# Kernel optimization log

Hardware: AMD Instinct MI355X
Metric: run time of the kernel (lower is better)

The kernel has to match this reference:

```python
import jax, jax.numpy as jnp
import numpy as np

N = 32768        # total nodes (B * max_num_nodes)
E = 524288       # edges, avg degree 16
F_ORI = 32       # data.x_ori feature dim
F_G = 32         # each gamora_output feature dim
IN = F_ORI + 3 * F_G  # 128
H = 256          # hidden_dim
OUT = 16         # out_dim
MAXN = 1024      # max_num_nodes
EPS = 1e-5       # BatchNorm eps


def setup_inputs() -> dict:
    key = jax.random.key(0)
    ks = list(jax.random.split(key, 32))
    g = lambda k, shape, fan: jax.random.normal(k, shape, jnp.float32) / np.sqrt(fan)
    inp = {}
    inp['x_ori'] = jax.random.normal(ks[0], (N, F_ORI), jnp.float32)
    inp['g0'] = jax.random.normal(ks[1], (N, F_G), jnp.float32)
    inp['g1'] = jax.random.normal(ks[2], (N, F_G), jnp.float32)
    inp['g2'] = jax.random.normal(ks[3], (N, F_G), jnp.float32)
    inp['edge_index'] = jax.random.randint(ks[4], (2, E), 0, N, jnp.int64)
    # SAGEConv layer 0: in_dim -> hidden
    inp['Wl0'] = g(ks[5], (IN, H), IN)
    inp['Wr0'] = g(ks[6], (IN, H), IN)
    inp['bb0'] = jnp.zeros((H,), jnp.float32)
    # SAGEConv layers 1..3: hidden -> hidden (stacked)
    inp['Wl'] = g(ks[7], (3, H, H), H)
    inp['Wr'] = g(ks[8], (3, H, H), H)
    inp['bb'] = jnp.zeros((3, H), jnp.float32)
    # BatchNorm per conv layer
    inp['gamma'] = jnp.ones((4, H), jnp.float32)
    inp['beta'] = jnp.zeros((4, H), jnp.float32)
    # mlp1: [max_num_nodes, hidden, 1]
    inp['W1a'] = g(ks[9], (MAXN, H), MAXN)
    inp['b1a'] = jnp.zeros((H,), jnp.float32)
    inp['W1b'] = g(ks[10], (H, 1), H)
    inp['b1b'] = jnp.zeros((1,), jnp.float32)
    # final BatchNorm
    inp['gamma_f'] = jnp.ones((H,), jnp.float32)
    inp['beta_f'] = jnp.zeros((H,), jnp.float32)
    # mlp2: [hidden, hidden, out_dim]
    inp['W2a'] = g(ks[11], (H, H), H)
    inp['b2a'] = jnp.zeros((H,), jnp.float32)
    inp['W2b'] = g(ks[12], (H, OUT), H)
    inp['b2b'] = jnp.zeros((OUT,), jnp.float32)
    return inp


def _bn(x, gamma, beta):
    # training-mode BatchNorm1d over the node/batch axis (biased variance)
    m = jnp.mean(x, axis=0)
    v = jnp.var(x, axis=0)
    return (x - m) * jax.lax.rsqrt(v + EPS) * gamma + beta


def _sage(x, src, dst, inv_deg, Wl, Wr, b):
    # mean neighbor aggregation (gather -> segment_sum -> normalize), then
    # out = lin_l(mean_agg) + lin_r(x)  (PyG SAGEConv, aggr='mean')
    agg = jax.ops.segment_sum(x[src], dst, num_segments=N)
    mean = agg * inv_deg[:, None]
    return mean @ Wl + x @ Wr + b


def reference(x_ori, g0, g1, g2, edge_index, Wl0, Wr0, bb0, Wl, Wr, bb,
              gamma, beta, W1a, b1a, W1b, b1b, gamma_f, beta_f,
              W2a, b2a, W2b, b2b):
    x = jnp.concatenate([x_ori, g0, g1, g2], axis=1)  # [N, IN]
    dst, src = edge_index[0], edge_index[1]
    deg = jax.ops.segment_sum(jnp.ones((E,), x.dtype), dst, num_segments=N)
    inv_deg = jnp.where(deg > 0, 1.0 / jnp.maximum(deg, 1.0), 0.0)
    # layer 0
    x = jax.nn.relu(_bn(_sage(x, src, dst, inv_deg, Wl0, Wr0, bb0), gamma[0], beta[0]))
    # layers 1..3 (dropout is identity in eval-mode reference)
    for i in range(3):
        x = jax.nn.relu(_bn(_sage(x, src, dst, inv_deg, Wl[i], Wr[i], bb[i]),
                            gamma[i + 1], beta[i + 1]))
    x = x.reshape(-1, H, MAXN)                 # [B, H, MAXN]
    h = jax.nn.relu(x @ W1a + b1a)             # [B, H, H]
    x = (h @ W1b + b1b).squeeze(2)             # [B, H]
    x = jax.nn.relu(_bn(x, gamma_f, beta_f))
    x = jax.nn.relu(x @ W2a + b2a) @ W2b + b2b  # [B, OUT]
    return x
```

## Files before the change

### kernel.cpp

```cpp
#include <hip/hip_runtime.h>

#define NN 32768
#define NE 524288
#define HD 256
#define TOTP 794897

#define GAS __attribute__((address_space(1)))
#define LAS __attribute__((address_space(3)))

typedef __attribute__((ext_vector_type(8))) __bf16 bf16x8;
typedef __attribute__((ext_vector_type(4))) float f32x4;

__device__ __forceinline__ float ld_any(const void* p, int i, int isbf16) {
    return isbf16 ? (float)((const __bf16*)p)[i] : ((const float*)p)[i];
}

struct PtrTable { const void* p[18]; };


__global__ __launch_bounds__(256) void k_pre(const unsigned* __restrict__ xw, const int* __restrict__ ei,
                                             PtrTable pt, const void* __restrict__ p0, const void* __restrict__ p1,
                                             const void* __restrict__ p2, const void* __restrict__ p3,
                                             int* __restrict__ flags, int* __restrict__ deg,
                                             __bf16* __restrict__ blob, __bf16* __restrict__ X0c) {
    __shared__ int fl[2];
    const int t = threadIdx.x;
    if (t < 64) {
        unsigned L = xw[t] & 0xFFFFu;
        int e = (int)((L >> 7) & 0xFF);
        unsigned long long b = __ballot(e >= 90 && e <= 135);
        if (t == 0) fl[0] = (b == ~0ULL) ? 1 : 0;
    } else if (t < 128) {
        int u = t - 64;
        unsigned long long b = __ballot(ei[2 * u + 1] != 0);
        if (t == 64) fl[1] = (b == 0ULL) ? 1 : 0;
    }
    __syncthreads();
    const int f0 = fl[0], f1 = fl[1];
    const int blk = blockIdx.x;
    if (blk == 0 && t < 2) flags[t] = fl[t];
    if (blk < 2048) {
        int i0 = (blk * 256 + t) * 8;
        int n = i0 >> 7, f = i0 & 127;
        const void* src = (f < 32) ? p0 : (f < 64) ? p1 : (f < 96) ? p2 : p3;
        int si = n * 32 + (f & 31);
        bf16x8 o;
        #pragma unroll
        for (int j = 0; j < 8; ++j) o[j] = (__bf16)ld_any(src, si + j, f0);
        *(bf16x8*)&X0c[i0] = o;
    } else if (blk < 3601) {
        const int off[23] = {0, 32768, 65536, 65792, 131328, 196864, 262400, 327936, 393472,
                             459008, 459776, 460800, 461824, 723968, 724224, 724480, 724481,
                             724737, 724993, 790529, 790785, 794881, TOTP};
        const signed char pidx[22] = {0, 1, 2, 3, 3, 3, 4, 4, 4, 5, 6, 7, 8, 9, 10, 11, 12, 13, 14, 15, 16, 17};
        const int sbase[22] = {0, 0, 0, 0, 65536, 131072, 0, 65536, 131072, 0, 0, 0, 0, 0, 0, 0, 0, 0, 0, 0, 0, 0};
        const signed char lR[22] = {7, 7, -1, 8, 8, 8, 8, 8, 8, -1, -1, -1, 10, -1, -1, -1, -1, -1, -1, -1, -1, -1};
        const signed char lC[22] = {8, 8, 0, 8, 8, 8, 8, 8, 8, 0, 0, 0, 8, 0, 0, 0, 0, 0, 0, 0, 0, 0};
        int base = ((blk - 2048) * 256 + t) * 2;
        #pragma unroll
        for (int j = 0; j < 2; ++j) {
            int i = base + j;
            if (i >= TOTP) break;
            int s = 0;
            while (i >= off[s + 1]) ++s;
            int jj = i - off[s];
            int si;
            if (lR[s] >= 0) {
                int Rm = (1 << lR[s]) - 1;
                si = sbase[s] + ((jj & Rm) << lC[s]) + (jj >> lR[s]);
            } else {
                si = sbase[s] + jj;
            }
            blob[i] = (__bf16)ld_any(pt.p[pidx[s]], si, f0);
        }
    } else {
        int e0 = ((blk - 3601) * 256 + t) * 2;
        int d0 = f1 ? ei[2 * e0] : ei[e0];
        int d1 = f1 ? ei[2 * e0 + 2] : ei[e0 + 1];
        atomicAdd(&deg[d0], 1);
        atomicAdd(&deg[d1], 1);
    }
}


__global__ __launch_bounds__(256) void k_alloc(const int* __restrict__ deg, int* __restrict__ gcur,
                                               int* __restrict__ offs, float* __restrict__ invd) {
    const int n = blockIdx.x * 256 + threadIdx.x;
    const int lane = threadIdx.x & 63;
    const int v = deg[n];
    invd[n] = v ? 1.f / (float)v : 0.f;
    int incl = v;
    #pragma unroll
    for (int d = 1; d < 64; d <<= 1) {
        int y = __shfl_up(incl, d, 64);
        if (lane >= d) incl += y;
    }
    int base = 0;
    if (lane == 63) base = atomicAdd(gcur, incl);
    base = __shfl(base, 63, 64);
    offs[n] = base + incl - v;
}

__global__ __launch_bounds__(256) void k_fill(const int* __restrict__ ei, const int* __restrict__ flags,
                                              const int* __restrict__ offs, int* __restrict__ cursor,
                                              int* __restrict__ csr) {
    int e = blockIdx.x * 256 + threadIdx.x;
    int f = flags[1];
    int d = f ? ei[2 * e] : ei[e];
    int s = f ? ei[2 * NE + 2 * e] : ei[NE + e];
    int p = atomicAdd(&cursor[d], 1);
    csr[offs[d] + p] = s;
}


__global__ __launch_bounds__(256) void k_agg0(const __bf16* __restrict__ X, const int* __restrict__ csr,
                                              const int* __restrict__ offs, const int* __restrict__ deg,
                                              const float* __restrict__ invd, __bf16* __restrict__ M) {
    const int t = threadIdx.x;
    const int s = blockIdx.x & 1;
    const int n = (blockIdx.x >> 1) * 32 + (t >> 3);
    const int fo = s * 64 + (t & 7) * 8;
    const int beg = offs[n], end = beg + deg[n];
    float a[8] = {};
    for (int e = beg; e < end; e += 8) {
        #pragma unroll
        for (int u = 0; u < 8; ++u) {
            int ee = e + u;
            int idx = csr[ee < end ? ee : end - 1] & (NN - 1);
            float mk = ee < end ? 1.f : 0.f;
            bf16x8 v = *(const bf16x8*)&X[(size_t)idx * 128 + fo];
            #pragma unroll
            for (int j = 0; j < 8; ++j) a[j] += mk * (float)v[j];
        }
    }
    const float id = invd[n];
    bf16x8 o;
    #pragma unroll
    for (int j = 0; j < 8; ++j) o[j] = (__bf16)(a[j] * id);
    *(bf16x8*)&M[(size_t)n * 128 + fo] = o;
}

__global__ __launch_bounds__(256) void k_agg(const __bf16* __restrict__ X, const int* __restrict__ csr,
                                             const int* __restrict__ offs, const int* __restrict__ deg,
                                             const float* __restrict__ invd, __bf16* __restrict__ M) {
    const int t = threadIdx.x;
    const int s = blockIdx.x & 3;
    const int n = (blockIdx.x >> 2) * 32 + (t >> 3);
    const int fo = s * 64 + (t & 7) * 8;
    const int beg = offs[n], end = beg + deg[n];
    float a[8] = {};
    for (int e = beg; e < end; e += 8) {
        #pragma unroll
        for (int u = 0; u < 8; ++u) {
            int ee = e + u;
            int idx = csr[ee < end ? ee : end - 1] & (NN - 1);
            float mk = ee < end ? 1.f : 0.f;
            bf16x8 v = *(const bf16x8*)&X[(size_t)idx * HD + fo];
            #pragma unroll
            for (int j = 0; j < 8; ++j) a[j] += mk * (float)v[j];
        }
    }
    const float id = invd[n];
    bf16x8 o;
    #pragma unroll
    for (int j = 0; j < 8; ++j) o[j] = (__bf16)(a[j] * id);
    *(bf16x8*)&M[(size_t)n * HD + fo] = o;
}


template <int MODE, int TM, int BNA>
__global__ __launch_bounds__(256) void k_gemm(const __bf16* __restrict__ A1, const __bf16* __restrict__ WT1,
                                              const __bf16* __restrict__ A2, const __bf16* __restrict__ WT2,
                                              const __bf16* __restrict__ bias, int KD,
                                              __bf16* __restrict__ O, float* __restrict__ colsum,
                                              const __bf16* __restrict__ W1b, float* __restrict__ x2,
                                              const float* __restrict__ pstatA, const __bf16* __restrict__ gA,
                                              const __bf16* __restrict__ bA) {
    constexpr int MI = TM / 32;
    __shared__ __bf16 As[2][TM][32];
    __shared__ __bf16 Bs[2][128][32];
    __shared__ float scs[256], shs[256];
    const int t = threadIdx.x;
    const int lane = t & 63, w = t >> 6;
    const int wm = w >> 1, wn = w & 1;
    const int quad = lane >> 4, l15 = lane & 15;
    const int row0 = blockIdx.x * TM, c0 = blockIdx.y * 128;
    const int dr = lane >> 2, dc = (lane & 3) * 8;
    if constexpr (BNA != 0) {
        const float invn = 1.0f / NN;
        float m = pstatA[t] * invn;
        float var = fmaxf(pstatA[256 + t] * invn - m * m, 0.f);
        float rs = rsqrtf(var + 1e-5f);
        float g = (float)gA[t] * rs;
        scs[t] = g;
        shs[t] = (float)bA[t] - m * g;
    }
    f32x4 acc[MI][4] = {};
    const int npass = A2 ? 2 : 1;
    for (int pass = 0; pass < npass; ++pass) {
        const __bf16* __restrict__ A = pass ? A2 : A1;
        const __bf16* __restrict__ WT = pass ? WT2 : WT1;
        for (int k0 = 0; k0 < KD; k0 += 64) {
            __syncthreads();
            #pragma unroll
            for (int kk = 0; kk < 2; ++kk) {
                #pragma unroll
                for (int i = 0; i < 2; ++i) {
                    const __bf16* g = &WT[(size_t)(c0 + w * 32 + i * 16 + dr) * KD + k0 + kk * 32 + dc];
                    __builtin_amdgcn_global_load_lds((const GAS void*)g, (LAS void*)&Bs[kk][w * 32 + i * 16][0],
                                                     16, 0, 0);
                }
                if ((BNA >> pass) & 1) {
                    const int kb = (k0 + kk * 32 + dc) & 255;
                    #pragma unroll
                    for (int i = 0; i < TM / 64; ++i) {
                        const __bf16* g = &A[(size_t)(row0 + w * (TM / 4) + i * 16 + dr) * KD + k0 + kk * 32 + dc];
                        bf16x8 v = *(const bf16x8*)g;
                        bf16x8 o;
                        #pragma unroll
                        for (int j = 0; j < 8; ++j)
                            o[j] = (__bf16)fmaxf((float)v[j] * scs[kb + j] + shs[kb + j], 0.f);
                        *(bf16x8*)&As[kk][w * (TM / 4) + i * 16 + dr][dc] = o;
                    }
                } else {
                    #pragma unroll
                    for (int i = 0; i < TM / 64; ++i) {
                        const __bf16* g = &A[(size_t)(row0 + w * (TM / 4) + i * 16 + dr) * KD + k0 + kk * 32 + dc];
                        __builtin_amdgcn_global_load_lds((const GAS void*)g,
                                                         (LAS void*)&As[kk][w * (TM / 4) + i * 16][0], 16, 0, 0);
                    }
                }
            }
            __syncthreads();
            #pragma unroll
            for (int kk = 0; kk < 2; ++kk) {
                bf16x8 af[MI], bfr[4];
                #pragma unroll
                for (int i = 0; i < MI; ++i) af[i] = *(const bf16x8*)&As[kk][wm * (TM / 2) + i * 16 + l15][quad * 8];
                #pragma unroll
                for (int j = 0; j < 4; ++j) bfr[j] = *(const bf16x8*)&Bs[kk][wn * 64 + j * 16 + l15][quad * 8];
                #pragma unroll
                for (int i = 0; i < MI; ++i)
                    #pragma unroll
                    for (int j = 0; j < 4; ++j)
                        acc[i][j] = __builtin_amdgcn_mfma_f32_16x16x32_bf16(af[i], bfr[j], acc[i][j], 0, 0, 0);
            }
        }
    }
    __syncthreads();
    if constexpr (MODE == 0) {
        float* lsum = (float*)&As[0][0][0];
        lsum[t] = 0.f;
        __syncthreads();
        #pragma unroll
        for (int j = 0; j < 4; ++j) {
            const int cb = wn * 64 + j * 16 + l15;
            const int col = c0 + cb;
            const float b = (float)bias[col];
            float s = 0.f, q = 0.f;
            #pragma unroll
            for (int i = 0; i < MI; ++i) {
                const size_t rbase = (size_t)(row0 + wm * (TM / 2) + i * 16 + quad * 4) * HD + col;
                #pragma unroll
                for (int r = 0; r < 4; ++r) {
                    float y = acc[i][j][r] + b;
                    O[rbase + (size_t)r * HD] = (__bf16)y;
                    s += y;
                    q += y * y;
                }
            }
            s += __shfl_xor(s, 16, 64); s += __shfl_xor(s, 32, 64);
            q += __shfl_xor(q, 16, 64); q += __shfl_xor(q, 32, 64);
            if (quad == 0) {
                atomicAdd(&lsum[cb], s);
                atomicAdd(&lsum[128 + cb], q);
            }
        }
        __syncthreads();
        if (t < 128) atomicAdd(&colsum[c0 + t], lsum[t]);
        else atomicAdd(&colsum[256 + c0 + t - 128], lsum[t]);
    } else {
        float bj[4], wj[4];
        #pragma unroll
        for (int j = 0; j < 4; ++j) {
            const int col = c0 + wn * 64 + j * 16 + l15;
            bj[j] = (float)bias[col];
            wj[j] = (float)W1b[col];
        }
        #pragma unroll
        for (int i = 0; i < MI; ++i) {
            #pragma unroll
            for (int r = 0; r < 4; ++r) {
                float p = 0.f;
                #pragma unroll
                for (int j = 0; j < 4; ++j) p += fmaxf(acc[i][j][r] + bj[j], 0.f) * wj[j];
                p += __shfl_xor(p, 1, 64); p += __shfl_xor(p, 2, 64);
                p += __shfl_xor(p, 4, 64); p += __shfl_xor(p, 8, 64);
                if (l15 == 0) atomicAdd(&x2[row0 + wm * (TM / 2) + i * 16 + quad * 4 + r], p);
            }
        }
    }
}


__global__ __launch_bounds__(256) void k_bnapply(__bf16* __restrict__ Y, const float* __restrict__ pstat,
                                                 const __bf16* __restrict__ gamma, const __bf16* __restrict__ beta) {
    __shared__ float sc[256], sh[256];
    const int t = threadIdx.x;
    {
        const float invn = 1.0f / NN;
        float m = pstat[t] * invn;
        float var = fmaxf(pstat[256 + t] * invn - m * m, 0.f);
        float rs = rsqrtf(var + 1e-5f);
        float s = (float)gamma[t] * rs;
        sc[t] = s;
        sh[t] = (float)beta[t] - m * s;
    }
    __syncthreads();
    size_t i = ((size_t)blockIdx.x * 256 + t) * 8;
    int c = (int)(i & 255);
    bf16x8 y = *(const bf16x8*)&Y[i];
    bf16x8 o;
    #pragma unroll
    for (int j = 0; j < 8; ++j) o[j] = (__bf16)fmaxf((float)y[j] * sc[c + j] + sh[c + j], 0.f);
    *(bf16x8*)&Y[i] = o;
}


__global__ __launch_bounds__(256) void k_mlp2(const float* __restrict__ x2, const __bf16* __restrict__ b1b,
                                              const __bf16* __restrict__ gf, const __bf16* __restrict__ bf_,
                                              const __bf16* __restrict__ W2a, const __bf16* __restrict__ b2a,
                                              const __bf16* __restrict__ W2b, const __bf16* __restrict__ b2b,
                                              const int* __restrict__ flags, void* __restrict__ out) {
    __shared__ float row[HD];
    __shared__ float hbuf[HD];
    __shared__ float part[256];
    const int b = blockIdx.x, t = threadIdx.x;
    const float b1 = (float)b1b[0];
    float s = 0.f, q = 0.f, mine = 0.f;
    #pragma unroll
    for (int r = 0; r < 32; ++r) {
        float v = x2[r * HD + t] + b1;
        s += v; q += v * v;
        if (r == b) mine = v;
    }
    float m = s * (1.0f / 32.0f);
    float var = fmaxf(q * (1.0f / 32.0f) - m * m, 0.f);
    float rs = rsqrtf(var + 1e-5f);
    float sc = (float)gf[t] * rs;
    float sh = (float)bf_[t] - m * sc;
    row[t] = fmaxf(mine * sc + sh, 0.f);
    __syncthreads();
    float acc = (float)b2a[t];
    for (int j = 0; j < HD; ++j) acc += row[j] * (float)W2a[j * HD + t];
    hbuf[t] = fmaxf(acc, 0.f);
    __syncthreads();
    const int k = t & 15, g = t >> 4;
    float p = 0.f;
    #pragma unroll
    for (int jj = 0; jj < 16; ++jj) p += hbuf[g * 16 + jj] * (float)W2b[(g * 16 + jj) * 16 + k];
    part[t] = p;
    __syncthreads();
    if (t < 16) {
        float o = (float)b2b[t];
        #pragma unroll
        for (int g2 = 0; g2 < 16; ++g2) o += part[g2 * 16 + t];
        if (flags[0]) ((__bf16*)out)[b * 16 + t] = (__bf16)o;
        else ((float*)out)[b * 16 + t] = o;
    }
}


extern "C" void kernel_launch(void* const* d_in, const int* in_sizes, int n_in,
                              void* d_out, int out_size, void* d_ws, size_t ws_size,
                              hipStream_t stream) {
    const int* ei = (const int*)d_in[4];

    char* ws = (char*)d_ws;
    size_t off_ = 0;
    auto ALLOC = [&](size_t b) { char* p = ws + off_; off_ += (b + 255) & ~(size_t)255; return p; };
    int* flags_ = (int*)ALLOC(8);
    size_t zbeg = off_;
    int* deg_ = (int*)ALLOC(NN * 4);
    int* cursor_ = (int*)ALLOC(NN * 4);
    float* colsum_ = (float*)ALLOC(4 * 512 * 4);
    float* x2_ = (float*)ALLOC(8192 * 4);
    int* gcur_ = (int*)ALLOC(4);
    size_t zlen = off_ - zbeg;
    int* offs_ = (int*)ALLOC(NN * 4);
    float* invd_ = (float*)ALLOC(NN * 4);
    int* csr_ = (int*)ALLOC((size_t)NE * 4);
    __bf16* blob_ = (__bf16*)ALLOC((size_t)TOTP * 2);
    __bf16* M_ = (__bf16*)ALLOC((size_t)NN * HD * 2);
    __bf16* Xa_ = (__bf16*)ALLOC((size_t)NN * HD * 2);
    __bf16* Xb_ = (__bf16*)ALLOC((size_t)NN * HD * 2);
    __bf16* X0c_ = Xb_;

    __bf16* Wl0T = blob_ + 0;
    __bf16* Wr0T = blob_ + 32768;
    __bf16* bb0c = blob_ + 65536;
    __bf16* WlT = blob_ + 65792;
    __bf16* WrT = blob_ + 262400;
    __bf16* bbc = blob_ + 459008;
    __bf16* gammac = blob_ + 459776;
    __bf16* betac = blob_ + 460800;
    __bf16* W1aT = blob_ + 461824;
    __bf16* b1ac = blob_ + 723968;
    __bf16* W1bc = blob_ + 724224;
    __bf16* b1bc = blob_ + 724480;
    __bf16* gfc = blob_ + 724481;
    __bf16* bfc = blob_ + 724737;
    __bf16* W2ac = blob_ + 724993;
    __bf16* b2ac = blob_ + 790529;
    __bf16* W2bc = blob_ + 790785;
    __bf16* b2bc = blob_ + 794881;

    PtrTable pt;
    pt.p[0] = d_in[5];  pt.p[1] = d_in[6];  pt.p[2] = d_in[7];  pt.p[3] = d_in[8];
    pt.p[4] = d_in[9];  pt.p[5] = d_in[10]; pt.p[6] = d_in[11]; pt.p[7] = d_in[12];
    pt.p[8] = d_in[13]; pt.p[9] = d_in[14]; pt.p[10] = d_in[15]; pt.p[11] = d_in[16];
    pt.p[12] = d_in[17]; pt.p[13] = d_in[18]; pt.p[14] = d_in[19]; pt.p[15] = d_in[20];
    pt.p[16] = d_in[21]; pt.p[17] = d_in[22];

    hipMemsetAsync(ws + zbeg, 0, zlen, stream);
    k_pre<<<4625, 256, 0, stream>>>((const unsigned*)d_in[0], ei, pt, d_in[0], d_in[1], d_in[2], d_in[3],
                                    flags_, deg_, blob_, X0c_);
    k_alloc<<<NN / 256, 256, 0, stream>>>(deg_, gcur_, offs_, invd_);
    k_fill<<<NE / 256, 256, 0, stream>>>(ei, flags_, offs_, cursor_, csr_);

    k_agg0<<<NN / 32 * 2, 256, 0, stream>>>(X0c_, csr_, offs_, deg_, invd_, M_);
    k_gemm<0, 128, 0><<<dim3(NN / 128, 2), 256, 0, stream>>>(M_, Wl0T, X0c_, Wr0T, bb0c, 128, Xa_, colsum_,
                                                             nullptr, nullptr, nullptr, nullptr, nullptr);
    k_bnapply<<<NN / 8, 256, 0, stream>>>(Xa_, colsum_, gammac, betac);

    __bf16* Xin = Xa_;
    __bf16* Xo = Xb_;
    for (int l = 0; l < 3; ++l) {
        float* cs = colsum_ + (l + 1) * 512;
        k_agg<<<NN / 32 * 4, 256, 0, stream>>>(Xin, csr_, offs_, deg_, invd_, M_);
        k_gemm<0, 128, 0><<<dim3(NN / 128, 2), 256, 0, stream>>>(M_, WlT + (size_t)l * HD * HD, Xin,
                                                                 WrT + (size_t)l * HD * HD, bbc + l * HD, 256, Xo,
                                                                 cs, nullptr, nullptr, nullptr, nullptr, nullptr);
        if (l < 2) k_bnapply<<<NN / 8, 256, 0, stream>>>(Xo, cs, gammac + (l + 1) * HD, betac + (l + 1) * HD);
        __bf16* tmp = Xin; Xin = Xo; Xo = tmp;
    }

    k_gemm<1, 64, 1><<<dim3(8192 / 64, 2), 256, 0, stream>>>(Xin, W1aT, nullptr, nullptr, b1ac, 1024, nullptr,
                                                             nullptr, W1bc, x2_, colsum_ + 3 * 512,
                                                             gammac + 3 * HD, betac + 3 * HD);
    k_mlp2<<<32, 256, 0, stream>>>(x2_, b1bc, gfc, bfc, W2ac, b2ac, W2bc, b2bc, flags_, d_out);
}
```

Before: 419.1 us.

## Spread edge gathers across wavefront lanes with padded CSR rows

The neighbor aggregation kernels now give each node a full wavefront: four edge groups of 16 lanes each gather 4-wide bf16 feature slices in parallel and combine them with cross-lane shuffles, instead of one 8-thread group walking edges serially. CSR row offsets are padded to multiples of 8 so that edge indices can be read with aligned int4 loads, and the CSR buffer is enlarged to fit the padding. This aims to raise memory-level parallelism and shorten the per-node serial chain. In exchange it launches eight times more blocks, issues smaller loads, and adds shuffle-reduction overhead.

```diff
diff --git a/kernel.cpp b/kernel.cpp
--- a/kernel.cpp
+++ b/kernel.cpp
@@ -9,6 +9,7 @@
 #define LAS __attribute__((address_space(3)))
 
 typedef __attribute__((ext_vector_type(8))) __bf16 bf16x8;
+typedef __attribute__((ext_vector_type(4))) __bf16 bf16x4;
 typedef __attribute__((ext_vector_type(4))) float f32x4;
 
 __device__ __forceinline__ float ld_any(const void* p, int i, int isbf16) {
@@ -89,7 +90,8 @@
     const int lane = threadIdx.x & 63;
     const int v = deg[n];
     invd[n] = v ? 1.f / (float)v : 0.f;
-    int incl = v;
+    const int v8 = (v + 7) & ~7;
+    int incl = v8;
     #pragma unroll
     for (int d = 1; d < 64; d <<= 1) {
         int y = __shfl_up(incl, d, 64);
@@ -98,7 +100,7 @@
     int base = 0;
     if (lane == 63) base = atomicAdd(gcur, incl);
     base = __shfl(base, 63, 64);
-    offs[n] = base + incl - v;
+    offs[n] = base + incl - v8;
 }
 
 __global__ __launch_bounds__(256) void k_fill(const int* __restrict__ ei, const int* __restrict__ flags,
@@ -118,26 +120,50 @@
                                               const float* __restrict__ invd, __bf16* __restrict__ M) {
     const int t = threadIdx.x;
     const int s = blockIdx.x & 1;
-    const int n = (blockIdx.x >> 1) * 32 + (t >> 3);
-    const int fo = s * 64 + (t & 7) * 8;
+    const int n = (blockIdx.x >> 1) * 4 + (t >> 6);
+    const int lane = t & 63;
+    const int eg = lane >> 4;
+    const int fo = s * 64 + (lane & 15) * 4;
     const int beg = offs[n], end = beg + deg[n];
-    float a[8] = {};
-    for (int e = beg; e < end; e += 8) {
-        #pragma unroll
-        for (int u = 0; u < 8; ++u) {
-            int ee = e + u;
-            int idx = csr[ee < end ? ee : end - 1] & (NN - 1);
-            float mk = ee < end ? 1.f : 0.f;
-            bf16x8 v = *(const bf16x8*)&X[(size_t)idx * 128 + fo];
-            #pragma unroll
-            for (int j = 0; j < 8; ++j) a[j] += mk * (float)v[j];
-        }
-    }
-    const float id = invd[n];
-    bf16x8 o;
-    #pragma unroll
-    for (int j = 0; j < 8; ++j) o[j] = (__bf16)(a[j] * id);
-    *(bf16x8*)&M[(size_t)n * 128 + fo] = o;
+    float a0 = 0.f, a1 = 0.f, a2 = 0.f, a3 = 0.f;
+    int e = beg;
+    for (; e + 8 <= end; e += 8) {
+        int4 c0 = *(const int4*)&csr[e];
+        int4 c1 = *(const int4*)&csr[e + 4];
+        int ia = ((eg == 0) ? c0.x : (eg == 1) ? c0.y : (eg == 2) ? c0.z : c0.w) & (NN - 1);
+        int ib = ((eg == 0) ? c1.x : (eg == 1) ? c1.y : (eg == 2) ? c1.z : c1.w) & (NN - 1);
+        bf16x4 va = *(const bf16x4*)&X[(size_t)ia * 128 + fo];
+        bf16x4 vb = *(const bf16x4*)&X[(size_t)ib * 128 + fo];
+        a0 += (float)va[0]; a1 += (float)va[1]; a2 += (float)va[2]; a3 += (float)va[3];
+        a0 += (float)vb[0]; a1 += (float)vb[1]; a2 += (float)vb[2]; a3 += (float)vb[3];
+    }
+    if (e + 4 <= end) {
+        int4 c0 = *(const int4*)&csr[e];
+        int ia = ((eg == 0) ? c0.x : (eg == 1) ? c0.y : (eg == 2) ? c0.z : c0.w) & (NN - 1);
+        bf16x4 va = *(const bf16x4*)&X[(size_t)ia * 128 + fo];
+        a0 += (float)va[0]; a1 += (float)va[1]; a2 += (float)va[2]; a3 += (float)va[3];
+        e += 4;
+    }
+    const int r = end - e;
+    if (r > 0) {
+        int ee = e + (eg < r ? eg : r - 1);
+        int idx = csr[ee] & (NN - 1);
+        float mk = eg < r ? 1.f : 0.f;
+        bf16x4 v = *(const bf16x4*)&X[(size_t)idx * 128 + fo];
+        a0 += mk * (float)v[0]; a1 += mk * (float)v[1];
+        a2 += mk * (float)v[2]; a3 += mk * (float)v[3];
+    }
+    a0 += __shfl_xor(a0, 16, 64); a0 += __shfl_xor(a0, 32, 64);
+    a1 += __shfl_xor(a1, 16, 64); a1 += __shfl_xor(a1, 32, 64);
+    a2 += __shfl_xor(a2, 16, 64); a2 += __shfl_xor(a2, 32, 64);
+    a3 += __shfl_xor(a3, 16, 64); a3 += __shfl_xor(a3, 32, 64);
+    if (eg == 0) {
+        const float id = invd[n];
+        bf16x4 o;
+        o[0] = (__bf16)(a0 * id); o[1] = (__bf16)(a1 * id);
+        o[2] = (__bf16)(a2 * id); o[3] = (__bf16)(a3 * id);
+        *(bf16x4*)&M[(size_t)n * 128 + fo] = o;
+    }
 }
 
 __global__ __launch_bounds__(256) void k_agg(const __bf16* __restrict__ X, const int* __restrict__ csr,
@@ -145,26 +171,50 @@
                                              const float* __restrict__ invd, __bf16* __restrict__ M) {
     const int t = threadIdx.x;
     const int s = blockIdx.x & 3;
-    const int n = (blockIdx.x >> 2) * 32 + (t >> 3);
-    const int fo = s * 64 + (t & 7) * 8;
+    const int n = (blockIdx.x >> 2) * 4 + (t >> 6);
+    const int lane = t & 63;
+    const int eg = lane >> 4;
+    const int fo = s * 64 + (lane & 15) * 4;
     const int beg = offs[n], end = beg + deg[n];
-    float a[8] = {};
-    for (int e = beg; e < end; e += 8) {
-        #pragma unroll
-        for (int u = 0; u < 8; ++u) {
-            int ee = e + u;
-            int idx = csr[ee < end ? ee : end - 1] & (NN - 1);
-            float mk = ee < end ? 1.f : 0.f;
-            bf16x8 v = *(const bf16x8*)&X[(size_t)idx * HD + fo];
-            #pragma unroll
-            for (int j = 0; j < 8; ++j) a[j] += mk * (float)v[j];
-        }
-    }
-    const float id = invd[n];
-    bf16x8 o;
-    #pragma unroll
-    for (int j = 0; j < 8; ++j) o[j] = (__bf16)(a[j] * id);
-    *(bf16x8*)&M[(size_t)n * HD + fo] = o;
+    float a0 = 0.f, a1 = 0.f, a2 = 0.f, a3 = 0.f;
+    int e = beg;
+    for (; e + 8 <= end; e += 8) {
+        int4 c0 = *(const int4*)&csr[e];
+        int4 c1 = *(const int4*)&csr[e + 4];
+        int ia = ((eg == 0) ? c0.x : (eg == 1) ? c0.y : (eg == 2) ? c0.z : c0.w) & (NN - 1);
+        int ib = ((eg == 0) ? c1.x : (eg == 1) ? c1.y : (eg == 2) ? c1.z : c1.w) & (NN - 1);
+        bf16x4 va = *(const bf16x4*)&X[(size_t)ia * HD + fo];
+        bf16x4 vb = *(const bf16x4*)&X[(size_t)ib * HD + fo];
+        a0 += (float)va[0]; a1 += (float)va[1]; a2 += (float)va[2]; a3 += (float)va[3];
+        a0 += (float)vb[0]; a1 += (float)vb[1]; a2 += (float)vb[2]; a3 += (float)vb[3];
+    }
+    if (e + 4 <= end) {
+        int4 c0 = *(const int4*)&csr[e];
+        int ia = ((eg == 0) ? c0.x : (eg == 1) ? c0.y : (eg == 2) ? c0.z : c0.w) & (NN - 1);
+        bf16x4 va = *(const bf16x4*)&X[(size_t)ia * HD + fo];
+        a0 += (float)va[0]; a1 += (float)va[1]; a2 += (float)va[2]; a3 += (float)va[3];
+        e += 4;
+    }
+    const int r = end - e;
+    if (r > 0) {
+        int ee = e + (eg < r ? eg : r - 1);
+        int idx = csr[ee] & (NN - 1);
+        float mk = eg < r ? 1.f : 0.f;
+        bf16x4 v = *(const bf16x4*)&X[(size_t)idx * HD + fo];
+        a0 += mk * (float)v[0]; a1 += mk * (float)v[1];
+        a2 += mk * (float)v[2]; a3 += mk * (float)v[3];
+    }
+    a0 += __shfl_xor(a0, 16, 64); a0 += __shfl_xor(a0, 32, 64);
+    a1 += __shfl_xor(a1, 16, 64); a1 += __shfl_xor(a1, 32, 64);
+    a2 += __shfl_xor(a2, 16, 64); a2 += __shfl_xor(a2, 32, 64);
+    a3 += __shfl_xor(a3, 16, 64); a3 += __shfl_xor(a3, 32, 64);
+    if (eg == 0) {
+        const float id = invd[n];
+        bf16x4 o;
+        o[0] = (__bf16)(a0 * id); o[1] = (__bf16)(a1 * id);
+        o[2] = (__bf16)(a2 * id); o[3] = (__bf16)(a3 * id);
+        *(bf16x4*)&M[(size_t)n * HD + fo] = o;
+    }
 }
 
 
@@ -389,7 +439,7 @@
     size_t zlen = off_ - zbeg;
     int* offs_ = (int*)ALLOC(NN * 4);
     float* invd_ = (float*)ALLOC(NN * 4);
-    int* csr_ = (int*)ALLOC((size_t)NE * 4);
+    int* csr_ = (int*)ALLOC(((size_t)NE + 8 * NN) * 4);
     __bf16* blob_ = (__bf16*)ALLOC((size_t)TOTP * 2);
     __bf16* M_ = (__bf16*)ALLOC((size_t)NN * HD * 2);
     __bf16* Xa_ = (__bf16*)ALLOC((size_t)NN * HD * 2);
@@ -428,7 +478,7 @@
     k_alloc<<<NN / 256, 256, 0, stream>>>(deg_, gcur_, offs_, invd_);
     k_fill<<<NE / 256, 256, 0, stream>>>(ei, flags_, offs_, cursor_, csr_);
 
-    k_agg0<<<NN / 32 * 2, 256, 0, stream>>>(X0c_, csr_, offs_, deg_, invd_, M_);
+    k_agg0<<<NN / 4 * 2, 256, 0, stream>>>(X0c_, csr_, offs_, deg_, invd_, M_);
     k_gemm<0, 128, 0><<<dim3(NN / 128, 2), 256, 0, stream>>>(M_, Wl0T, X0c_, Wr0T, bb0c, 128, Xa_, colsum_,
                                                              nullptr, nullptr, nullptr, nullptr, nullptr);
     k_bnapply<<<NN / 8, 256, 0, stream>>>(Xa_, colsum_, gammac, betac);
@@ -437,7 +487,7 @@
     __bf16* Xo = Xb_;
     for (int l = 0; l < 3; ++l) {
         float* cs = colsum_ + (l + 1) * 512;
-        k_agg<<<NN / 32 * 4, 256, 0, stream>>>(Xin, csr_, offs_, deg_, invd_, M_);
+        k_agg<<<NN / 4 * 4, 256, 0, stream>>>(Xin, csr_, offs_, deg_, invd_, M_);
         k_gemm<0, 128, 0><<<dim3(NN / 128, 2), 256, 0, stream>>>(M_, WlT + (size_t)l * HD * HD, Xin,
                                                                  WrT + (size_t)l * HD * HD, bbc + l * HD, 256, Xo,
                                                                  cs, nullptr, nullptr, nullptr, nullptr, nullptr);
```

New measurement: 555.9 us. +32.6%, slower.
